# Performance work log

Measured on AMD Instinct MI355X. Metric: run time of the kernel, lower is better.

## Reference

```python
import jax, jax.numpy as jnp
import numpy as np

B, S, D, H, F, E, K = 2, 2048, 1024, 16, 4096, 8, 2
DH = D // H
EPS = 1e-6  # RMSNorm eps (torch nn.RMSNorm default ~ fp32 machine eps; 1e-6 used here)


def _rmsnorm(x, w):
    return x * jax.lax.rsqrt(jnp.mean(x * x, axis=-1, keepdims=True) + EPS) * w


def setup_inputs() -> dict:
    key = jax.random.key(0)
    ks = jax.random.split(key, 16)
    std = 0.02
    return {
        "x": jax.random.normal(ks[0], (B, S, D), jnp.float32),
        "norm1_w": jnp.ones((D,), jnp.float32),
        "norm2_w": jnp.ones((D,), jnp.float32),
        "w_qkv": jax.random.normal(ks[1], (D, 3 * D), jnp.float32) * std,
        "b_qkv": jnp.zeros((3 * D,), jnp.float32),
        "w_o": jax.random.normal(ks[2], (D, D), jnp.float32) * std,
        "b_o": jnp.zeros((D,), jnp.float32),
        "router_w": jax.random.normal(ks[3], (D, E), jnp.float32) * std,
        "router_b": jnp.zeros((E,), jnp.float32),
        "w1": jax.random.normal(ks[4], (E, D, F), jnp.float32) * std,
        "b1": jnp.zeros((E, F), jnp.float32),
        "w2": jax.random.normal(ks[5], (E, F, D), jnp.float32) * std,
        "b2": jnp.zeros((E, D), jnp.float32),
    }


def reference(x, norm1_w, norm2_w, w_qkv, b_qkv, w_o, b_o,
              router_w, router_b, w1, b1, w2, b2):
    # ---- pre-norm causal multi-head attention ----
    h = _rmsnorm(x, norm1_w)
    qkv = h @ w_qkv + b_qkv                                  # [B,S,3D]
    q, k, v = jnp.split(qkv, 3, axis=-1)
    q = q.reshape(B, S, H, DH).transpose(0, 2, 1, 3)         # [B,H,S,DH]
    k = k.reshape(B, S, H, DH).transpose(0, 2, 1, 3)
    v = v.reshape(B, S, H, DH).transpose(0, 2, 1, 3)
    scores = jnp.einsum('bhqd,bhkd->bhqk', q, k) / jnp.sqrt(jnp.asarray(DH, x.dtype))
    causal = jnp.tril(jnp.ones((S, S), bool))
    scores = jnp.where(causal, scores, jnp.asarray(-1e9, x.dtype))
    attn = jax.nn.softmax(scores, axis=-1)
    ao = jnp.einsum('bhqk,bhkd->bhqd', attn, v).transpose(0, 2, 1, 3).reshape(B, S, D)
    x = x + (ao @ w_o + b_o)

    # ---- pre-norm top-k MoE feed-forward ----
    h2 = _rmsnorm(x, norm2_w)
    t = h2.reshape(-1, D)                                    # [T,D], T=B*S
    logits = t @ router_w + router_b                         # [T,E]
    probs = jax.nn.softmax(logits, axis=-1)
    topv, topi = jax.lax.top_k(probs, K)                     # [T,K]
    gates_k = topv / jnp.sum(topv, axis=-1, keepdims=True)   # renormalized top-k gates
    oh = jax.nn.one_hot(topi, E, dtype=x.dtype)              # [T,K,E]
    gates = jnp.einsum('tke,tk->te', oh, gates_k)            # dense gates, zero off top-k

    out = jnp.zeros_like(t)
    for e in range(E):                                       # fixed small expert loop
        he = jax.nn.gelu(t @ w1[e] + b1[e], approximate=False)
        ye = he @ w2[e] + b2[e]
        out = out + gates[:, e:e + 1] * ye

    # load-balancing aux loss: E * sum_e f_e * P_e
    f = jnp.mean(jnp.sum(oh, axis=1), axis=0)                # fraction routed to each expert
    P = jnp.mean(probs, axis=0)                              # mean router prob per expert
    aux_loss = jnp.asarray(E, x.dtype) * jnp.sum(f * P)

    x = x + out.reshape(B, S, D)
    return (x, aux_loss)
```

## Files before the change

### kernel.cpp

```cpp
#include <hip/hip_runtime.h>
#include <math.h>

#define TB 2
#define TS 2048
#define TD 1024
#define TH 16
#define TDH 64
#define TF 4096
#define TE 8
#define TT 4096
#define PSTR (TB*TH*TS*TDH)

typedef __attribute__((ext_vector_type(8))) __bf16 bf16x8;
typedef __attribute__((ext_vector_type(4))) float f32x4;
typedef __attribute__((ext_vector_type(8))) short short8;
typedef __attribute__((ext_vector_type(4))) unsigned short ushort4v;
typedef __attribute__((ext_vector_type(4))) float fvec4;

__device__ inline unsigned short f2bf(float f) {
  union { float f; unsigned int u; } v; v.f = f;
  unsigned int u = v.u;
  unsigned int r = (u + 0x7FFFu + ((u >> 16) & 1u)) >> 16;
  return (unsigned short)r;
}
__device__ inline float bf2f(unsigned short h) {
  union { unsigned int u; float f; } v; v.u = ((unsigned int)h) << 16; return v.f;
}
__device__ inline void split2(float x, unsigned short& h, unsigned short& m) {
  h = f2bf(x);
  m = f2bf(x - bf2f(h));
}

__device__ inline f32x4 mfma_bf16(short8 a, short8 b, f32x4 c) {
  return __builtin_amdgcn_mfma_f32_16x16x32_bf16(
      __builtin_bit_cast(bf16x8, a), __builtin_bit_cast(bf16x8, b), c, 0, 0, 0);
}

__device__ inline void gload16(const void* g, void* l) {
  __builtin_amdgcn_global_load_lds(
      (const __attribute__((address_space(1))) void*)g,
      (__attribute__((address_space(3))) void*)l, 16, 0, 0);
}

__device__ inline float gelu_f(float v) {
  float ax = fabsf(v) * 0.70710678118654752f;
  float t = __builtin_amdgcn_rcpf(1.0f + 0.3275911f * ax);
  float poly = ((((1.061405429f * t - 1.453152027f) * t + 1.421413741f) * t
                 - 0.284496736f) * t + 0.254829592f) * t;
  float er = 1.0f - poly * __expf(-ax * ax);
  er = copysignf(er, v);
  return 0.5f * v * (1.0f + er);
}

__global__ __launch_bounds__(256)
void tcvt_kernel(const float* __restrict__ In, unsigned short* __restrict__ Out,
                 int R, int C) {
  __shared__ float tile[32][33];
  In  += (size_t)blockIdx.z * R * C;
  Out += (size_t)blockIdx.z * R * C;
  int c0 = blockIdx.x * 32, r0 = blockIdx.y * 32;
  int tx = threadIdx.x & 31, ty = threadIdx.x >> 5;
#pragma unroll
  for (int i = 0; i < 4; ++i)
    tile[ty + 8*i][tx] = In[(size_t)(r0 + ty + 8*i) * C + c0 + tx];
  __syncthreads();
#pragma unroll
  for (int i = 0; i < 4; ++i)
    Out[(size_t)(c0 + ty + 8*i) * R + r0 + tx] = f2bf(tile[tx][ty + 8*i]);
}

__global__ __launch_bounds__(256)
void tcvt_split_kernel(const float* __restrict__ In,
                       unsigned short* __restrict__ O0,
                       unsigned short* __restrict__ O1, int R, int C) {
  __shared__ float tile[32][33];
  int c0 = blockIdx.x * 32, r0 = blockIdx.y * 32;
  int tx = threadIdx.x & 31, ty = threadIdx.x >> 5;
#pragma unroll
  for (int i = 0; i < 4; ++i)
    tile[ty + 8*i][tx] = In[(size_t)(r0 + ty + 8*i) * C + c0 + tx];
  __syncthreads();
#pragma unroll
  for (int i = 0; i < 4; ++i) {
    float v = tile[tx][ty + 8*i];
    unsigned short h, m; split2(v, h, m);
    size_t idx = (size_t)(c0 + ty + 8*i) * R + r0 + tx;
    O0[idx] = h; O1[idx] = m;
  }
}

__global__ __launch_bounds__(256)
void rmsnorm_kernel(const float* __restrict__ X, const float* __restrict__ W,
                    unsigned short* __restrict__ O) {
  int row = blockIdx.x;
  int tid = threadIdx.x;
  int lane = tid & 63, wave = tid >> 6;
  const float* xr = X + (size_t)row * TD;
  fvec4 v = *(const fvec4*)(xr + tid * 4);
  float ss = v[0]*v[0] + v[1]*v[1] + v[2]*v[2] + v[3]*v[3];
#pragma unroll
  for (int msk = 1; msk < 64; msk <<= 1) ss += __shfl_xor(ss, msk);
  __shared__ float red[4];
  if (lane == 0) red[wave] = ss;
  __syncthreads();
  ss = red[0] + red[1] + red[2] + red[3];
  float rs = rsqrtf(ss * (1.0f / TD) + 1e-6f);
  fvec4 wv = *(const fvec4*)(W + tid * 4);
  ushort4v o;
#pragma unroll
  for (int j = 0; j < 4; ++j) o[j] = f2bf(v[j] * rs * wv[j]);
  *(ushort4v*)(O + (size_t)row * TD + tid * 4) = o;
}

__global__ __launch_bounds__(256)
void rmsnorm_split_kernel(const float* __restrict__ X, const float* __restrict__ W,
                          unsigned short* __restrict__ O0,
                          unsigned short* __restrict__ O1) {
  int row = blockIdx.x;
  int tid = threadIdx.x;
  int lane = tid & 63, wave = tid >> 6;
  const float* xr = X + (size_t)row * TD;
  fvec4 v = *(const fvec4*)(xr + tid * 4);
  float ss = v[0]*v[0] + v[1]*v[1] + v[2]*v[2] + v[3]*v[3];
#pragma unroll
  for (int msk = 1; msk < 64; msk <<= 1) ss += __shfl_xor(ss, msk);
  __shared__ float red[4];
  if (lane == 0) red[wave] = ss;
  __syncthreads();
  ss = red[0] + red[1] + red[2] + red[3];
  float rs = rsqrtf(ss * (1.0f / TD) + 1e-6f);
  fvec4 wv = *(const fvec4*)(W + tid * 4);
  ushort4v o0, o1;
#pragma unroll
  for (int j = 0; j < 4; ++j) {
    unsigned short h, m; split2(v[j] * rs * wv[j], h, m);
    o0[j] = h; o1[j] = m;
  }
  size_t idx = (size_t)row * TD + tid * 4;
  *(ushort4v*)(O0 + idx) = o0;
  *(ushort4v*)(O1 + idx) = o1;
}

template<int MODE>
__global__ __launch_bounds__(256)
void gemm2(const unsigned short* __restrict__ A0,
           const unsigned short* __restrict__ A1,
           const unsigned short* __restrict__ B0,
           const unsigned short* __restrict__ B1,
           const float* __restrict__ bias, int Kd,
           float* __restrict__ outF, const float* __restrict__ resid,
           unsigned short* __restrict__ S0,
           unsigned short* __restrict__ S1) {
  __shared__ __align__(16) unsigned short As0[2][4096], As1[2][4096];
  __shared__ __align__(16) unsigned short Bs0[2][4096], Bs1[2][4096];
  const int tid = threadIdx.x;
  const int lane = tid & 63;
  const int w = tid >> 6;
  const int wr = w >> 1, wc = w & 1;
  const int g = lane >> 4;
  const int l15 = lane & 15;
  const int m0 = blockIdx.y * 128;
  const int n0 = blockIdx.x * 128;

  const int c_swz = (lane & 3) ^ ((lane >> 3) & 3);
  const unsigned short *a0p[2], *a1p[2], *b0p[2], *b1p[2];
  int ldsrow[2];
#pragma unroll
  for (int j = 0; j < 2; ++j) {
    int r16 = w * 2 + j;
    int r = r16 * 16 + (lane >> 2);
    a0p[j] = A0 + (size_t)(m0 + r) * Kd + c_swz * 8;
    a1p[j] = A1 + (size_t)(m0 + r) * Kd + c_swz * 8;
    b0p[j] = B0 + (size_t)(n0 + r) * Kd + c_swz * 8;
    b1p[j] = B1 + (size_t)(n0 + r) * Kd + c_swz * 8;
    ldsrow[j] = r16 * 512;
  }

#define G2_STAGE(p, koff)                              \
  {                                                    \
    _Pragma("unroll")                                  \
    for (int j = 0; j < 2; ++j) {                      \
      gload16(a0p[j] + (koff), &As0[p][ldsrow[j]]);    \
      gload16(a1p[j] + (koff), &As1[p][ldsrow[j]]);    \
      gload16(b0p[j] + (koff), &Bs0[p][ldsrow[j]]);    \
      gload16(b1p[j] + (koff), &Bs1[p][ldsrow[j]]);    \
    }                                                  \
  }

  f32x4 acc[4][4] = {};
  const int nt = Kd >> 5;

  G2_STAGE(0, 0);
  for (int t = 0; t < nt; ++t) {
    const int p = t & 1;
    if (t + 1 < nt) {
      G2_STAGE(p ^ 1, (t + 1) * 32);
      asm volatile("s_waitcnt vmcnt(8)" ::: "memory");
    } else {
      asm volatile("s_waitcnt vmcnt(0)" ::: "memory");
    }
    __builtin_amdgcn_s_barrier();

    short8 a0f[4], a1f[4], b0f[4], b1f[4];
#pragma unroll
    for (int mi = 0; mi < 4; ++mi) {
      int row = wr * 64 + mi * 16 + l15;
      int off = (row * 64 + g * 16) ^ (((row >> 1) & 3) << 4);
      a0f[mi] = *(const short8*)((const char*)As0[p] + off);
      a1f[mi] = *(const short8*)((const char*)As1[p] + off);
    }
#pragma unroll
    for (int ni = 0; ni < 4; ++ni) {
      int row = wc * 64 + ni * 16 + l15;
      int off = (row * 64 + g * 16) ^ (((row >> 1) & 3) << 4);
      b0f[ni] = *(const short8*)((const char*)Bs0[p] + off);
      b1f[ni] = *(const short8*)((const char*)Bs1[p] + off);
    }
#pragma unroll
    for (int mi = 0; mi < 4; ++mi)
#pragma unroll
      for (int ni = 0; ni < 4; ++ni) {
        f32x4 tacc = acc[mi][ni];
        tacc = mfma_bf16(a0f[mi], b0f[ni], tacc);
        tacc = mfma_bf16(a0f[mi], b1f[ni], tacc);
        tacc = mfma_bf16(a1f[mi], b0f[ni], tacc);
        acc[mi][ni] = tacc;
      }
    __builtin_amdgcn_s_barrier();
  }
#undef G2_STAGE

#pragma unroll
  for (int mi = 0; mi < 4; ++mi) {
#pragma unroll
    for (int ni = 0; ni < 4; ++ni) {
      int n = n0 + wc * 64 + ni * 16 + l15;
      float bv = bias[n];
      if (MODE == 0) {
        int part = n >> 10, d = n & 1023, hh = d >> 6, dh = d & 63;
        int s0r = m0 + wr * 64 + mi * 16 + g * 4;
        int b = s0r >> 11, s_ = s0r & 2047;
        int bh = b * TH + hh;
        if (part < 2) {
          size_t base = (size_t)part * PSTR + (size_t)bh * (TS * TDH) + (size_t)s_ * TDH + dh;
#pragma unroll
          for (int r = 0; r < 4; ++r) {
            unsigned short h, m; split2(acc[mi][ni][r] + bv, h, m);
            size_t idx = base + (size_t)r * TDH;
            S0[idx] = h; S1[idx] = m;
          }
        } else {
          ushort4v o0, o1;
#pragma unroll
          for (int r = 0; r < 4; ++r) {
            unsigned short h, m; split2(acc[mi][ni][r] + bv, h, m);
            o0[r] = h; o1[r] = m;
          }
          size_t idx = 2 * (size_t)PSTR + (size_t)bh * (TS * TDH) + (size_t)dh * TS + s_;
          *(ushort4v*)(S0 + idx) = o0;
          *(ushort4v*)(S1 + idx) = o1;
        }
      } else {
#pragma unroll
        for (int r = 0; r < 4; ++r) {
          int m = m0 + wr * 64 + mi * 16 + g * 4 + r;
          size_t idx = (size_t)m * TD + n;
          outF[idx] = acc[mi][ni][r] + bv + resid[idx];
        }
      }
    }
  }
}

__global__ __launch_bounds__(512, 4)
void attn2_kernel(const unsigned short* __restrict__ S0,
                  const unsigned short* __restrict__ S1,
                  unsigned short* __restrict__ A0,
                  unsigned short* __restrict__ A1) {
  __shared__ __align__(16) char Kt0[8192], Kt1[8192];
  __shared__ __align__(16) char Vt0[8192], Vt1[8192];
  __shared__ __align__(16) char Pt0[16384], Pt1[16384];

  const int tid = threadIdx.x;
  const int lane = tid & 63;
  const int wave = tid >> 6;
  const int g = lane >> 4, l15 = lane & 15;

  const int bh = blockIdx.y;
  const int b = bh >> 4, hh = bh & 15;

  const size_t qbase = (size_t)bh * TS * TDH;
  const size_t kbase = (size_t)PSTR + qbase;
  const size_t vbase = 2 * (size_t)PSTR + qbase;

  for (int half = 0; half < 2; ++half) {
    const int qtb = half ? (15 - (int)blockIdx.x) : (int)blockIdx.x;
    const int qlo = qtb * 128 + wave * 16;

    short8 aq0[2], aq1[2];
#pragma unroll
    for (int c = 0; c < 2; ++c) {
      size_t qo = qbase + (size_t)(qlo + l15) * TDH + c * 32 + g * 8;
      aq0[c] = *(const short8*)(S0 + qo);
      aq1[c] = *(const short8*)(S1 + qo);
    }

    f32x4 accv[4] = {};
    float m_[4] = {-1e30f, -1e30f, -1e30f, -1e30f};
    float l_[4] = {0.f, 0.f, 0.f, 0.f};

    const int ktmax = 2 * qtb + 1;
    for (int kt = 0; kt <= ktmax; ++kt) {
      __syncthreads();
      {
        int row = tid >> 3, ch = tid & 7;
        int off = (row * 128 + ch * 16) ^ ((row & 7) << 4);
        size_t kg = kbase + (size_t)(kt * 64 + row) * TDH + ch * 8;
        *(short8*)(Kt0 + off) = *(const short8*)(S0 + kg);
        *(short8*)(Kt1 + off) = *(const short8*)(S1 + kg);
        size_t vg = vbase + (size_t)row * TS + kt * 64 + ch * 8;
        *(short8*)(Vt0 + off) = *(const short8*)(S0 + vg);
        *(short8*)(Vt1 + off) = *(const short8*)(S1 + vg);
      }
      __syncthreads();

      if (kt * 64 > qlo + 15) continue;
      const bool needmask = (kt * 64 + 63 > qlo);

      f32x4 sf[4] = {};
#pragma unroll
      for (int kb = 0; kb < 4; ++kb) {
#pragma unroll
        for (int c = 0; c < 2; ++c) {
          int krow = kb * 16 + l15;
          int off = (krow * 128 + (c * 32 + g * 8) * 2) ^ ((krow & 7) << 4);
          short8 bk0 = *(const short8*)(Kt0 + off);
          short8 bk1 = *(const short8*)(Kt1 + off);
          f32x4 t = sf[kb];
          t = mfma_bf16(aq0[c], bk0, t);
          t = mfma_bf16(aq0[c], bk1, t);
          t = mfma_bf16(aq1[c], bk0, t);
          sf[kb] = t;
        }
      }

      float pv[4][4];
#pragma unroll
      for (int r = 0; r < 4; ++r) {
        float s0 = sf[0][r] * 0.125f, s1 = sf[1][r] * 0.125f;
        float s2 = sf[2][r] * 0.125f, s3 = sf[3][r] * 0.125f;
        if (needmask) {
          int qg = qlo + g * 4 + r;
          int k0g = kt * 64 + l15;
          if (k0g      > qg) s0 = -1e30f;
          if (k0g + 16 > qg) s1 = -1e30f;
          if (k0g + 32 > qg) s2 = -1e30f;
          if (k0g + 48 > qg) s3 = -1e30f;
        }
        float mx = fmaxf(fmaxf(s0, s1), fmaxf(s2, s3));
#pragma unroll
        for (int msk = 1; msk < 16; msk <<= 1) mx = fmaxf(mx, __shfl_xor(mx, msk));
        float nm = fmaxf(m_[r], mx);
        float sc = __expf(m_[r] - nm);
        float p0 = __expf(s0 - nm), p1 = __expf(s1 - nm);
        float p2 = __expf(s2 - nm), p3 = __expf(s3 - nm);
        float rs = p0 + p1 + p2 + p3;
#pragma unroll
        for (int msk = 1; msk < 16; msk <<= 1) rs += __shfl_xor(rs, msk);
        m_[r] = nm;
        l_[r] = l_[r] * sc + rs;
#pragma unroll
        for (int dhb = 0; dhb < 4; ++dhb) accv[dhb][r] *= sc;
        pv[0][r] = p0; pv[1][r] = p1; pv[2][r] = p2; pv[3][r] = p3;
      }

      char* P0 = Pt0 + wave * 2048;
      char* P1 = Pt1 + wave * 2048;
#pragma unroll
      for (int kb = 0; kb < 4; ++kb) {
#pragma unroll
        for (int r = 0; r < 4; ++r) {
          int prow = g * 4 + r;
          int key = kb * 16 + l15;
          int off = (prow * 128 + key * 2) ^ ((prow & 7) << 4);
          unsigned short h, m; split2(pv[kb][r], h, m);
          *(unsigned short*)(P0 + off) = h;
          *(unsigned short*)(P1 + off) = m;
        }
      }
      short8 pa0[2], pa1[2];
#pragma unroll
      for (int c = 0; c < 2; ++c) {
        int off = (l15 * 128 + (c * 32 + g * 8) * 2) ^ ((l15 & 7) << 4);
        pa0[c] = *(const short8*)(P0 + off);
        pa1[c] = *(const short8*)(P1 + off);
      }
#pragma unroll
      for (int dhb = 0; dhb < 4; ++dhb) {
#pragma unroll
        for (int c = 0; c < 2; ++c) {
          int dh = dhb * 16 + l15;
          int off = (dh * 128 + (c * 32 + g * 8) * 2) ^ ((dh & 7) << 4);
          short8 bv0 = *(const short8*)(Vt0 + off);
          short8 bv1 = *(const short8*)(Vt1 + off);
          f32x4 t = accv[dhb];
          t = mfma_bf16(pa0[c], bv0, t);
          t = mfma_bf16(pa0[c], bv1, t);
          t = mfma_bf16(pa1[c], bv0, t);
          accv[dhb] = t;
        }
      }
    }

#pragma unroll
    for (int dhb = 0; dhb < 4; ++dhb) {
#pragma unroll
      for (int r = 0; r < 4; ++r) {
        int srow = qlo + g * 4 + r;
        int col = hh * 64 + dhb * 16 + l15;
        unsigned short h, m; split2(accv[dhb][r] / l_[r], h, m);
        size_t idx = ((size_t)(b * TS + srow)) * TD + col;
        A0[idx] = h; A1[idx] = m;
      }
    }
  }
}

__global__ __launch_bounds__(256)
void moe_gather_kernel(const unsigned short* __restrict__ h2,
                       const int* __restrict__ tperm,
                       unsigned short* __restrict__ h2p) {
  int slot = blockIdx.x;
  int t = tperm[slot];
  const ushort4v* src = (const ushort4v*)(h2 + (size_t)t * TD);
  ushort4v* dst = (ushort4v*)(h2p + (size_t)slot * TD);
  dst[threadIdx.x] = src[threadIdx.x];
}

template<int MODE>
__global__ __launch_bounds__(256)
void gemm_bt(const unsigned short* __restrict__ A,
             const unsigned short* __restrict__ Bt,
             const float* __restrict__ bias,
             int N, int Kd,
             float* __restrict__ ysl,
             unsigned short* __restrict__ outH,
             const int* __restrict__ seg_off,
             const int* __restrict__ seg_cnt,
             const float* __restrict__ gate_perm) {
  __shared__ __align__(16) unsigned short As[2][4096];
  __shared__ __align__(16) unsigned short Bs[2][4096];

  const int tid = threadIdx.x;
  const int lane = tid & 63;
  const int w = tid >> 6;
  const int wr = w >> 1, wc = w & 1;
  const int g = lane >> 4;
  const int l15 = lane & 15;

  const int e = blockIdx.z;
  const int m0 = blockIdx.y * 128;
  const int n0 = blockIdx.x * 128;
  const int off = seg_off[e];
  const int Mrows = seg_cnt[e];
  if (m0 >= Mrows) return;
  Bt += (size_t)e * N * Kd;
  bias += (size_t)e * N;

  const int c_swz = (lane & 3) ^ ((lane >> 3) & 3);
  const unsigned short* aptr[2];
  const unsigned short* bptr[2];
  int ldsrow[2];
#pragma unroll
  for (int j = 0; j < 2; ++j) {
    int r16 = w * 2 + j;
    int r = r16 * 16 + (lane >> 2);
    int rc = (m0 + r < Mrows) ? (m0 + r) : (Mrows - 1);
    aptr[j] = A + (size_t)(off + rc) * Kd + c_swz * 8;
    bptr[j] = Bt + (size_t)(n0 + r) * Kd + c_swz * 8;
    ldsrow[j] = r16 * 512;
  }

#define GB_STAGE(p, koff)                           \
  {                                                 \
    _Pragma("unroll")                               \
    for (int j = 0; j < 2; ++j) {                   \
      gload16(aptr[j] + (koff), &As[p][ldsrow[j]]); \
      gload16(bptr[j] + (koff), &Bs[p][ldsrow[j]]); \
    }                                               \
  }

  f32x4 acc[4][4] = {};
  const int nt = Kd >> 5;

  GB_STAGE(0, 0);
  for (int t = 0; t < nt; ++t) {
    const int p = t & 1;
    if (t + 1 < nt) {
      GB_STAGE(p ^ 1, (t + 1) * 32);
      asm volatile("s_waitcnt vmcnt(4)" ::: "memory");
    } else {
      asm volatile("s_waitcnt vmcnt(0)" ::: "memory");
    }
    __builtin_amdgcn_s_barrier();

    short8 af[4], bfr[4];
#pragma unroll
    for (int mi = 0; mi < 4; ++mi) {
      int row = wr * 64 + mi * 16 + l15;
      int o2 = (row * 64 + g * 16) ^ (((row >> 1) & 3) << 4);
      af[mi] = *(const short8*)((const char*)As[p] + o2);
    }
#pragma unroll
    for (int ni = 0; ni < 4; ++ni) {
      int row = wc * 64 + ni * 16 + l15;
      int o2 = (row * 64 + g * 16) ^ (((row >> 1) & 3) << 4);
      bfr[ni] = *(const short8*)((const char*)Bs[p] + o2);
    }
#pragma unroll
    for (int mi = 0; mi < 4; ++mi)
#pragma unroll
      for (int ni = 0; ni < 4; ++ni)
        acc[mi][ni] = mfma_bf16(af[mi], bfr[ni], acc[mi][ni]);
    __builtin_amdgcn_s_barrier();
  }
#undef GB_STAGE

#pragma unroll
  for (int mi = 0; mi < 4; ++mi) {
#pragma unroll
    for (int ni = 0; ni < 4; ++ni) {
      int n = n0 + wc * 64 + ni * 16 + l15;
      float bv = bias[n];
#pragma unroll
      for (int r = 0; r < 4; ++r) {
        int mloc = m0 + wr * 64 + mi * 16 + g * 4 + r;
        if (mloc >= Mrows) continue;
        float val = acc[mi][ni][r] + bv;
        if (MODE == 2) {
          outH[(size_t)(off + mloc) * TF + n] = f2bf(gelu_f(val));
        } else {
          float gv = gate_perm[off + mloc];
          ysl[(size_t)(off + mloc) * TD + n] = gv * val;
        }
      }
    }
  }
}

__global__ __launch_bounds__(256)
void moe_reduce_kernel(const float* __restrict__ ys, const int* __restrict__ tslot,
                       float* __restrict__ out) {
  int t = blockIdx.x;
  int d = threadIdx.x * 4;
  fvec4 a = *(const fvec4*)(ys + (size_t)tslot[t * 2] * TD + d);
  fvec4 b = *(const fvec4*)(ys + (size_t)tslot[t * 2 + 1] * TD + d);
  float* o = out + (size_t)t * TD + d;
  fvec4 c = *(const fvec4*)o;
#pragma unroll
  for (int j = 0; j < 4; ++j) c[j] += a[j] + b[j];
  *(fvec4*)o = c;
}

__global__ __launch_bounds__(256)
void router_kernel(const float* __restrict__ X1, const float* __restrict__ N2W,
                   const float* __restrict__ RW, const float* __restrict__ RB,
                   int* __restrict__ top_e, float* __restrict__ top_g,
                   int* __restrict__ counts, float* __restrict__ p_sum) {
  __shared__ float s_psum[TE];
  __shared__ int s_cnt[TE];
  if (threadIdx.x < TE) { s_psum[threadIdx.x] = 0.f; s_cnt[threadIdx.x] = 0; }
  __syncthreads();
  int lane = threadIdx.x & 63, wave = threadIdx.x >> 6;
  for (int it = 0; it < 16; ++it) {
    int t = (blockIdx.x * 4 + wave) * 16 + it;
    const float* xr = X1 + (size_t)t * TD;
    float vals[16]; float ss = 0.f;
#pragma unroll
    for (int i = 0; i < 16; ++i) { float xv = xr[i * 64 + lane]; vals[i] = xv; ss += xv * xv; }
#pragma unroll
    for (int msk = 1; msk < 64; msk <<= 1) ss += __shfl_xor(ss, msk);
    float rs = rsqrtf(ss * (1.0f / TD) + 1e-6f);
    float acc[TE] = {};
#pragma unroll
    for (int i = 0; i < 16; ++i) {
      int d = i * 64 + lane;
      float nv = vals[i] * rs * N2W[d];
      const float* rwp = RW + (size_t)d * TE;
#pragma unroll
      for (int e2 = 0; e2 < TE; ++e2) acc[e2] += nv * rwp[e2];
    }
#pragma unroll
    for (int msk = 1; msk < 64; msk <<= 1)
#pragma unroll
      for (int e2 = 0; e2 < TE; ++e2) acc[e2] += __shfl_xor(acc[e2], msk);
    if (lane == 0) {
      float lg[TE]; float mx = -1e30f;
      for (int e2 = 0; e2 < TE; ++e2) { lg[e2] = acc[e2] + RB[e2]; mx = fmaxf(mx, lg[e2]); }
      float sum = 0.f, pe[TE];
      for (int e2 = 0; e2 < TE; ++e2) { pe[e2] = expf(lg[e2] - mx); sum += pe[e2]; }
      float inv = 1.0f / sum;
      for (int e2 = 0; e2 < TE; ++e2) atomicAdd(&s_psum[e2], pe[e2] * inv);
      int i1 = 0;
      for (int e2 = 1; e2 < TE; ++e2) if (lg[e2] > lg[i1]) i1 = e2;
      int i2 = (i1 == 0) ? 1 : 0;
      for (int e2 = 0; e2 < TE; ++e2) if (e2 != i1 && lg[e2] > lg[i2]) i2 = e2;
      float g1 = pe[i1], g2 = pe[i2], gs = g1 + g2;
      top_e[t * 2] = i1; top_e[t * 2 + 1] = i2;
      top_g[t * 2] = g1 / gs; top_g[t * 2 + 1] = g2 / gs;
      atomicAdd(&s_cnt[i1], 1); atomicAdd(&s_cnt[i2], 1);
    }
  }
  __syncthreads();
  if (threadIdx.x < TE) {
    atomicAdd(&p_sum[threadIdx.x], s_psum[threadIdx.x]);
    atomicAdd(&counts[threadIdx.x], s_cnt[threadIdx.x]);
  }
}

__global__ void zero_meta_kernel(int* counts, float* p_sum) {
  int t = threadIdx.x;
  if (t < TE) { counts[t] = 0; p_sum[t] = 0.f; }
}

__global__ void offsets_kernel(const int* counts, int* offs, int* cursor) {
  if (threadIdx.x == 0) {
    int o = 0;
    for (int e2 = 0; e2 < TE; ++e2) { offs[e2] = o; o += counts[e2]; }
  }
  if (threadIdx.x < TE) cursor[threadIdx.x] = 0;
}

__global__ __launch_bounds__(256)
void fill_kernel(const int* __restrict__ top_e, const float* __restrict__ top_g,
                 const int* __restrict__ offs, int* __restrict__ cursor,
                 int* __restrict__ token_perm, float* __restrict__ gate_perm,
                 int* __restrict__ tslot) {
  __shared__ int s_cnt[TE], s_base[TE];
  if (threadIdx.x < TE) s_cnt[threadIdx.x] = 0;
  __syncthreads();
  int t = blockIdx.x * 256 + threadIdx.x;
  int e0 = top_e[t * 2], e1 = top_e[t * 2 + 1];
  int r0 = atomicAdd(&s_cnt[e0], 1);
  int r1 = atomicAdd(&s_cnt[e1], 1);
  __syncthreads();
  if (threadIdx.x < TE)
    s_base[threadIdx.x] = atomicAdd(&cursor[threadIdx.x], s_cnt[threadIdx.x]);
  __syncthreads();
  int p0 = offs[e0] + s_base[e0] + r0;
  int p1 = offs[e1] + s_base[e1] + r1;
  token_perm[p0] = t; gate_perm[p0] = top_g[t * 2];
  token_perm[p1] = t; gate_perm[p1] = top_g[t * 2 + 1];
  tslot[t * 2] = p0; tslot[t * 2 + 1] = p1;
}

__global__ void aux_kernel(const int* counts, const float* p_sum, float* outv) {
  if (threadIdx.x == 0) {
    float a = 0.f;
    for (int e2 = 0; e2 < TE; ++e2)
      a += ((float)counts[e2] / (float)TT) * (p_sum[e2] / (float)TT);
    outv[0] = (float)TE * a;
  }
}

extern "C" void kernel_launch(void* const* d_in, const int* in_sizes, int n_in,
                              void* d_out, int out_size, void* d_ws, size_t ws_size,
                              hipStream_t stream) {
  const float* x     = (const float*)d_in[0];
  const float* n1w   = (const float*)d_in[1];
  const float* n2w   = (const float*)d_in[2];
  const float* w_qkv = (const float*)d_in[3];
  const float* b_qkv = (const float*)d_in[4];
  const float* w_o   = (const float*)d_in[5];
  const float* b_o   = (const float*)d_in[6];
  const float* rw    = (const float*)d_in[7];
  const float* rb    = (const float*)d_in[8];
  const float* w1    = (const float*)d_in[9];
  const float* b1    = (const float*)d_in[10];
  const float* w2    = (const float*)d_in[11];
  const float* b2    = (const float*)d_in[12];
  float* out = (float*)d_out;
  char* ws = (char*)d_ws;

  size_t o = 0;
  auto give = [&](size_t bytes) -> char* {
    char* p = ws + o;
    o += (bytes + 255) & ~(size_t)255;
    return p;
  };
  unsigned short* w1T = (unsigned short*)give(8ull * 4096 * 1024 * 2);
  unsigned short* w2T = (unsigned short*)give(8ull * 1024 * 4096 * 2);
  unsigned short* wo0 = (unsigned short*)give(1024ull * 1024 * 2);
  unsigned short* wo1 = (unsigned short*)give(1024ull * 1024 * 2);
  unsigned short* h2  = (unsigned short*)give((size_t)TT * TD * 2);
  int*   counts = (int*)give(TE * 4);
  int*   cursor = (int*)give(TE * 4);
  int*   offs   = (int*)give(TE * 4);
  float* psum   = (float*)give(TE * 4);
  int*   top_e  = (int*)give(2ull * TT * 4);
  float* top_g  = (float*)give(2ull * TT * 4);
  int*   tperm  = (int*)give(2ull * TT * 4);
  float* gperm  = (float*)give(2ull * TT * 4);
  int*   tslot  = (int*)give(2ull * TT * 4);
  unsigned short* wq0 = (unsigned short*)give(3072ull * 1024 * 2);
  unsigned short* wq1 = (unsigned short*)give(3072ull * 1024 * 2);
  float* ys = (float*)give(2ull * TT * TD * 4);
  char* poolB = give(2ull * TT * TD * 2);
  unsigned short* h10 = (unsigned short*)poolB;
  unsigned short* h11 = (unsigned short*)(poolB + (size_t)TT * TD * 2);
  unsigned short* ao0 = h10; unsigned short* ao1 = h11;
  unsigned short* h2p = (unsigned short*)poolB;
  char* poolC = give(64ull * 1024 * 1024);
  unsigned short* qs0 = (unsigned short*)poolC;
  unsigned short* qs1 = (unsigned short*)(poolC + 3ull * PSTR * 2);
  unsigned short* he  = (unsigned short*)poolC;

  tcvt_split_kernel<<<dim3(96, 32, 1), 256, 0, stream>>>(w_qkv, wq0, wq1, 1024, 3072);
  tcvt_split_kernel<<<dim3(32, 32, 1), 256, 0, stream>>>(w_o, wo0, wo1, 1024, 1024);
  tcvt_kernel<<<dim3(128, 32, 8), 256, 0, stream>>>(w1, w1T, 1024, 4096);
  tcvt_kernel<<<dim3(32, 128, 8), 256, 0, stream>>>(w2, w2T, 4096, 1024);

  rmsnorm_split_kernel<<<dim3(TT), 256, 0, stream>>>(x, n1w, h10, h11);
  gemm2<0><<<dim3(24, 32, 1), 256, 0, stream>>>(
      h10, h11, wq0, wq1, b_qkv, 1024, nullptr, nullptr, qs0, qs1);
  attn2_kernel<<<dim3(8, 32, 1), 512, 0, stream>>>(qs0, qs1, ao0, ao1);
  gemm2<1><<<dim3(8, 32, 1), 256, 0, stream>>>(
      ao0, ao1, wo0, wo1, b_o, 1024, out, x, nullptr, nullptr);

  rmsnorm_kernel<<<dim3(TT), 256, 0, stream>>>(out, n2w, h2);
  zero_meta_kernel<<<dim3(1), 64, 0, stream>>>(counts, psum);
  router_kernel<<<dim3(64), 256, 0, stream>>>(out, n2w, rw, rb, top_e, top_g, counts, psum);
  offsets_kernel<<<dim3(1), 64, 0, stream>>>(counts, offs, cursor);
  fill_kernel<<<dim3(TT / 256), 256, 0, stream>>>(top_e, top_g, offs, cursor, tperm, gperm, tslot);
  moe_gather_kernel<<<dim3(2 * TT), 256, 0, stream>>>(h2, tperm, h2p);
  gemm_bt<2><<<dim3(32, 32, 8), 256, 0, stream>>>(
      h2p, w1T, b1, 4096, 1024, nullptr, he, offs, counts, gperm);
  gemm_bt<3><<<dim3(8, 32, 8), 256, 0, stream>>>(
      he, w2T, b2, 1024, 4096, ys, nullptr, offs, counts, gperm);
  moe_reduce_kernel<<<dim3(TT), 256, 0, stream>>>(ys, tslot, out);
  aux_kernel<<<dim3(1), 64, 0, stream>>>(counts, psum, out + (size_t)TT * TD);
}
```

Baseline: 744.2 us.

## Use 256x256 tiles with 8 waves for the MoE up-projection GEMM

Replaces the templated 128x128 grouped GEMM for the expert up-projection (with fused GELU) with a dedicated 512-thread kernel using 256x256 output tiles. Each wave computes 128x64 with a K=64 double-buffered LDS pipeline and XOR-swizzled reads. The larger tile raises arithmetic intensity and cuts global reloads of A and B. In exchange it uses 128KB of LDS and many accumulator registers, which limits occupancy. It also wastes more work on padded rows in partially filled expert segments, and with fewer blocks the GPU's CUs may be underfilled.

```diff
diff --git a/kernel.cpp b/kernel.cpp
--- a/kernel.cpp
+++ b/kernel.cpp
@@ -437,14 +437,112 @@
   dst[threadIdx.x] = src[threadIdx.x];
 }
 
-template<int MODE>
-__global__ __launch_bounds__(256)
-void gemm_bt(const unsigned short* __restrict__ A,
+__global__ __launch_bounds__(512)
+void gemm_up8(const unsigned short* __restrict__ A,
+              const unsigned short* __restrict__ Bt,
+              const float* __restrict__ bias,
+              int N, int Kd,
+              unsigned short* __restrict__ outH,
+              const int* __restrict__ seg_off,
+              const int* __restrict__ seg_cnt) {
+  __shared__ __align__(16) unsigned short As[2][256 * 64];
+  __shared__ __align__(16) unsigned short Bs[2][256 * 64];
+
+  const int tid = threadIdx.x;
+  const int lane = tid & 63;
+  const int w = tid >> 6;
+  const int wm = w >> 2, wn = w & 3;
+  const int g = lane >> 4;
+  const int l15 = lane & 15;
+
+  const int e = blockIdx.z;
+  const int m0 = blockIdx.y * 256;
+  const int n0 = blockIdx.x * 256;
+  const int off = seg_off[e];
+  const int Mrows = seg_cnt[e];
+  if (m0 >= Mrows) return;
+  Bt += (size_t)e * N * Kd;
+  bias += (size_t)e * N;
+
+  const int gc = (lane & 7) ^ ((lane >> 3) & 7);
+  const unsigned short* aptr[4];
+  const unsigned short* bptr[4];
+#pragma unroll
+  for (int rnd = 0; rnd < 4; ++rnd) {
+    int rl = rnd * 64 + w * 8 + (lane >> 3);
+    int rc = (m0 + rl < Mrows) ? (m0 + rl) : (Mrows - 1);
+    aptr[rnd] = A + (size_t)(off + rc) * Kd + gc * 8;
+    bptr[rnd] = Bt + (size_t)(n0 + rl) * Kd + gc * 8;
+  }
+
+#define UP8_STAGE(p, koff)                                        \
+  {                                                               \
+    _Pragma("unroll")                                             \
+    for (int rnd = 0; rnd < 4; ++rnd) {                           \
+      gload16(aptr[rnd] + (koff), &As[p][(rnd * 64 + w * 8) * 64]); \
+      gload16(bptr[rnd] + (koff), &Bs[p][(rnd * 64 + w * 8) * 64]); \
+    }                                                             \
+  }
+
+  f32x4 acc[8][4] = {};
+  const int nt = Kd >> 6;
+
+  UP8_STAGE(0, 0);
+  __syncthreads();
+
+  for (int t = 0; t < nt; ++t) {
+    const int p = t & 1;
+    if (t + 1 < nt) UP8_STAGE(p ^ 1, (t + 1) * 64);
+
+#pragma unroll
+    for (int ph = 0; ph < 4; ++ph) {
+      const int mh = ph >> 1, kk = ph & 1;
+      short8 af[4], bfr[4];
+#pragma unroll
+      for (int q = 0; q < 4; ++q) {
+        int row = wm * 128 + (mh * 4 + q) * 16 + l15;
+        int o2 = row * 128 + ((((kk << 2) | g) ^ (row & 7)) << 4);
+        af[q] = *(const short8*)((const char*)As[p] + o2);
+      }
+#pragma unroll
+      for (int ni = 0; ni < 4; ++ni) {
+        int row = wn * 64 + ni * 16 + l15;
+        int o2 = row * 128 + ((((kk << 2) | g) ^ (row & 7)) << 4);
+        bfr[ni] = *(const short8*)((const char*)Bs[p] + o2);
+      }
+#pragma unroll
+      for (int q = 0; q < 4; ++q)
+#pragma unroll
+        for (int ni = 0; ni < 4; ++ni)
+          acc[mh * 4 + q][ni] = mfma_bf16(af[q], bfr[ni], acc[mh * 4 + q][ni]);
+    }
+    __syncthreads();
+  }
+#undef UP8_STAGE
+
+#pragma unroll
+  for (int mi = 0; mi < 8; ++mi) {
+#pragma unroll
+    for (int ni = 0; ni < 4; ++ni) {
+      int n = n0 + wn * 64 + ni * 16 + l15;
+      float bv = bias[n];
+#pragma unroll
+      for (int r = 0; r < 4; ++r) {
+        int mloc = m0 + wm * 128 + mi * 16 + g * 4 + r;
+        if (mloc >= Mrows) continue;
+        float val = acc[mi][ni][r] + bv;
+        outH[(size_t)(off + mloc) * TF + n] = f2bf(gelu_f(val));
+      }
+    }
+  }
+}
+
+__global__ __launch_bounds__(256)
+void gemm_dn(const unsigned short* __restrict__ A,
              const unsigned short* __restrict__ Bt,
              const float* __restrict__ bias,
              int N, int Kd,
              float* __restrict__ ysl,
-             unsigned short* __restrict__ outH,
              const int* __restrict__ seg_off,
              const int* __restrict__ seg_cnt,
              const float* __restrict__ gate_perm) {
@@ -537,12 +635,8 @@
         int mloc = m0 + wr * 64 + mi * 16 + g * 4 + r;
         if (mloc >= Mrows) continue;
         float val = acc[mi][ni][r] + bv;
-        if (MODE == 2) {
-          outH[(size_t)(off + mloc) * TF + n] = f2bf(gelu_f(val));
-        } else {
-          float gv = gate_perm[off + mloc];
-          ysl[(size_t)(off + mloc) * TD + n] = gv * val;
-        }
+        float gv = gate_perm[off + mloc];
+        ysl[(size_t)(off + mloc) * TD + n] = gv * val;
       }
     }
   }
@@ -733,10 +827,10 @@
   offsets_kernel<<<dim3(1), 64, 0, stream>>>(counts, offs, cursor);
   fill_kernel<<<dim3(TT / 256), 256, 0, stream>>>(top_e, top_g, offs, cursor, tperm, gperm, tslot);
   moe_gather_kernel<<<dim3(2 * TT), 256, 0, stream>>>(h2, tperm, h2p);
-  gemm_bt<2><<<dim3(32, 32, 8), 256, 0, stream>>>(
-      h2p, w1T, b1, 4096, 1024, nullptr, he, offs, counts, gperm);
-  gemm_bt<3><<<dim3(8, 32, 8), 256, 0, stream>>>(
-      he, w2T, b2, 1024, 4096, ys, nullptr, offs, counts, gperm);
+  gemm_up8<<<dim3(16, 16, 8), 512, 0, stream>>>(
+      h2p, w1T, b1, 4096, 1024, he, offs, counts);
+  gemm_dn<<<dim3(8, 32, 8), 256, 0, stream>>>(
+      he, w2T, b2, 1024, 4096, ys, offs, counts, gperm);
   moe_reduce_kernel<<<dim3(TT), 256, 0, stream>>>(ys, tslot, out);
   aux_kernel<<<dim3(1), 64, 0, stream>>>(counts, psum, out + (size_t)TT * TD);
 }
```

Measured after the change: 756.9 us. About the same (+1.7%).
